# Optimization experiments

Measured on AMD Instinct MI355X. Metric: run time of the kernel, lower is better.

Reference implementation:

```python
import jax, jax.numpy as jnp
import numpy as np

B, S, D, H, FF = 2, 2048, 1024, 16, 4096
DK = D // H
MAX_SEQ_LEN = 2048
THETA = 10000.0
EPS = 1e-5


def _linear_init(key, out_f, in_f):
    std = (2.0 / (in_f + out_f)) ** 0.5
    return std * jax.random.truncated_normal(key, -3.0, 3.0, (out_f, in_f), dtype=jnp.float32)


def setup_inputs() -> dict:
    key = jax.random.key(0)
    ks = jax.random.split(key, 9)
    x = jax.random.normal(ks[0], (B, S, D), dtype=jnp.float32)
    token_positions = jnp.broadcast_to(jnp.arange(S, dtype=jnp.int32)[None, :], (B, S))
    return {
        "x": x,
        "wq": _linear_init(ks[1], D, D),
        "wk": _linear_init(ks[2], D, D),
        "wv": _linear_init(ks[3], D, D),
        "wo": _linear_init(ks[4], D, D),
        "w1": _linear_init(ks[5], FF, D),
        "w2": _linear_init(ks[6], D, FF),
        "w3": _linear_init(ks[7], FF, D),
        "g1": jnp.ones((D,), dtype=jnp.float32),
        "g2": jnp.ones((D,), dtype=jnp.float32),
        "token_positions": token_positions,
    }


def _rmsnorm(x, g):
    x32 = x.astype(jnp.float32)
    ms = jnp.sqrt(jnp.mean(x32 * x32, axis=-1, keepdims=True) + EPS)
    return ((x32 / ms) * g).astype(x.dtype)


def _rope(x, pos):
    # x: (B, H, S, DK); pos: (B, S)
    inv_freq = 1.0 / THETA ** (jnp.arange(0, DK, 2, dtype=jnp.float32) / DK)  # (DK/2,)
    freqs = pos.astype(jnp.float32)[..., None] * inv_freq  # (B, S, DK/2)
    cos = jnp.cos(freqs)[:, None, :, :]  # (B, 1, S, DK/2) broadcast over heads
    sin = jnp.sin(freqs)[:, None, :, :]
    x_real = x[..., 0::2]
    x_imag = x[..., 1::2]
    rot_real = x_real * cos - x_imag * sin
    rot_imag = x_real * sin + x_imag * cos
    return jnp.stack([rot_real, rot_imag], axis=-1).reshape(x.shape)


def reference(x, wq, wk, wv, wo, w1, w2, w3, g1, g2, token_positions):
    # --- attention sublayer ---
    h = _rmsnorm(x, g1)
    def proj(w):
        y = jnp.einsum('bsd,ed->bse', h, w)
        return y.reshape(B, S, H, DK).transpose(0, 2, 1, 3)  # (B,H,S,DK)
    Q = _rope(proj(wq), token_positions)
    K = _rope(proj(wk), token_positions)
    V = proj(wv)
    scores = jnp.einsum('bhqd,bhkd->bhqk', Q, K)  # (B,H,S,S) full matrix (naive)
    causal = jnp.tril(jnp.ones((S, S), dtype=bool))
    scores = jnp.where(causal, scores, -jnp.inf) / (DK ** 0.5)
    probs = jax.nn.softmax(scores, axis=-1)
    attn = jnp.einsum('bhqk,bhkd->bhqd', probs, V)
    attn = attn.transpose(0, 2, 1, 3).reshape(B, S, D)
    attn = jnp.einsum('bsd,ed->bse', attn, wo)
    y = x + attn
    # --- SwiGLU FFN sublayer ---
    h2 = _rmsnorm(y, g2)
    a = jnp.einsum('bsd,fd->bsf', h2, w1)
    gate = jnp.einsum('bsd,fd->bsf', h2, w3)
    ff = jnp.einsum('bsf,df->bsd', a * jax.nn.sigmoid(a) * gate, w2)
    return y + ff
```

## Files before the change

### kernel.cpp

```cpp
#include <hip/hip_runtime.h>
#include <hip/hip_bf16.h>

#define B_ 2
#define S_ 2048
#define D_ 1024
#define H_ 16
#define DK_ 64
#define FF_ 4096
#define M_ (B_ * S_)

typedef unsigned short u16;
typedef __bf16 bf16x8 __attribute__((ext_vector_type(8)));
typedef float f32x4 __attribute__((ext_vector_type(4)));
typedef u16 u16x4 __attribute__((ext_vector_type(4)));
typedef u16 u16x8 __attribute__((ext_vector_type(8)));

__device__ __forceinline__ u16 f2bf(float f) {
  __bf16 b = (__bf16)f;
  return __builtin_bit_cast(u16, b);
}
__device__ __forceinline__ float bf2f(u16 u) {
  __bf16 b = __builtin_bit_cast(__bf16, u);
  return (float)b;
}

__device__ __forceinline__ void async_lds16(const void* g, void* l) {
  __builtin_amdgcn_global_load_lds(
      (const __attribute__((address_space(1))) unsigned int*)g,
      (__attribute__((address_space(3))) unsigned int*)l, 16, 0, 0);
}

__device__ __forceinline__ void raw_barrier() {
  asm volatile("s_barrier" ::: "memory");
}
#define VMCNT_WAIT(n) asm volatile("s_waitcnt vmcnt(" #n ")" ::: "memory")

__global__ __launch_bounds__(256) void f2b_all(
    const float* __restrict__ wq, const float* __restrict__ wk,
    const float* __restrict__ wv, const float* __restrict__ wo,
    const float* __restrict__ w1, const float* __restrict__ w2,
    const float* __restrict__ w3, u16* __restrict__ wqkvb,
    u16* __restrict__ wob, u16* __restrict__ wb13, u16* __restrict__ w2b) {
  int i4 = blockIdx.x * 256 + threadIdx.x;
  const float* src;
  u16* dst;
  int off, oo;
  if (i4 < 262144) { src = wq; dst = wqkvb; off = i4; oo = off; }
  else if (i4 < 524288) { src = wk; dst = wqkvb + 1048576; off = i4 - 262144; oo = off; }
  else if (i4 < 786432) { src = wv; dst = wqkvb + 2097152; off = i4 - 524288; oo = off; }
  else if (i4 < 1048576) { src = wo; dst = wob; off = i4 - 786432; oo = off; }
  else if (i4 < 2097152) {
    src = w1; dst = wb13; off = i4 - 1048576;
    oo = ((off >> 8) * 2) * 256 + (off & 255);
  } else if (i4 < 3145728) { src = w2; dst = w2b; off = i4 - 2097152; oo = off; }
  else {
    src = w3; dst = wb13; off = i4 - 3145728;
    oo = ((off >> 8) * 2 + 1) * 256 + (off & 255);
  }
  float4 v = ((const float4*)src)[off];
  u16x4 o;
  o[0] = f2bf(v.x); o[1] = f2bf(v.y); o[2] = f2bf(v.z); o[3] = f2bf(v.w);
  *(u16x4*)(dst + (size_t)oo * 4) = o;
}

__global__ __launch_bounds__(256) void rmsnorm_k(const float* __restrict__ X,
                                                 const float* __restrict__ G,
                                                 u16* __restrict__ Out) {
  const int row = blockIdx.x, tid = threadIdx.x;
  const float4 xv = *(const float4*)(X + (size_t)row * D_ + tid * 4);
  float ss = xv.x * xv.x + xv.y * xv.y + xv.z * xv.z + xv.w * xv.w;
#pragma unroll
  for (int off = 1; off < 64; off <<= 1) ss += __shfl_xor(ss, off);
  __shared__ float red[4];
  if ((tid & 63) == 0) red[tid >> 6] = ss;
  __syncthreads();
  const float tot = red[0] + red[1] + red[2] + red[3];
  const float sc = rsqrtf(tot * (1.0f / D_) + 1e-5f);
  const float4 gv = *(const float4*)(G + tid * 4);
  u16x4 o;
  o[0] = f2bf(xv.x * sc * gv.x);
  o[1] = f2bf(xv.y * sc * gv.y);
  o[2] = f2bf(xv.z * sc * gv.z);
  o[3] = f2bf(xv.w * sc * gv.w);
  *(u16x4*)(Out + (size_t)row * D_ + tid * 4) = o;
}

__global__ __launch_bounds__(256) void rope2_k(unsigned int* __restrict__ Qb,
                                               unsigned int* __restrict__ Kb,
                                               const int* __restrict__ pos) {
  int idx = blockIdx.x * 256 + threadIdx.x;
  unsigned int* buf = Qb;
  float scale = 0.125f;
  if (idx >= 2097152) { buf = Kb; scale = 1.f; idx -= 2097152; }
  const int row = idx >> 9, p = idx & 511;
  const int i = p & 31;
  unsigned int v = buf[(size_t)row * 512 + p];
  const float xr = bf2f((u16)(v & 0xffffu));
  const float xi = bf2f((u16)(v >> 16));
  const float ang =
      (float)pos[row] * __expf(-(float)i * (9.210340371976184f / 32.0f));
  float sn, cs;
  sincosf(ang, &sn, &cs);
  const float orr = (xr * cs - xi * sn) * scale;
  const float oii = (xr * sn + xi * cs) * scale;
  buf[(size_t)row * 512 + p] =
      (unsigned int)f2bf(orr) | ((unsigned int)f2bf(oii) << 16);
}

__global__ __launch_bounds__(256) void transpose_v(const u16* __restrict__ V,
                                                   u16* __restrict__ Vt) {
  __shared__ __align__(16) u16 tile[32][64];
  const int tid = threadIdx.x;
  const int s0 = blockIdx.x * 32, bh = blockIdx.y, b = bh >> 4, h = bh & 15;
  {
    const int sr = tid >> 3, c = tid & 7;
    *(u16x8*)&tile[sr][c * 8] =
        *(const u16x8*)(V + (size_t)(b * S_ + s0 + sr) * D_ + h * DK_ + c * 8);
  }
  __syncthreads();
  {
    const int dk = tid >> 2, cs = tid & 3;
    u16x8 vv;
#pragma unroll
    for (int j = 0; j < 8; ++j) vv[j] = tile[cs * 8 + j][dk];
    *(u16x8*)(Vt + (size_t)(bh * DK_ + dk) * S_ + s0 + cs * 8) = vv;
  }
}

template <int EPI>
__global__ __launch_bounds__(512) void gemm8ph(const u16* __restrict__ A,
                                               const u16* __restrict__ Bw,
                                               void* __restrict__ Cout,
                                               const void* __restrict__ auxp,
                                               int N, int K) {
  constexpr int BM = 256, BN = 256, BK = 64;
  constexpr int CPR = BK / 8;
  constexpr int ACH = BM * CPR;
  __shared__ __align__(16) u16 As[2][BM * BK];
  __shared__ __align__(16) u16 Bs[2][BN * BK];
  const int tid = threadIdx.x, l = tid & 63, w = tid >> 6;
  const int gx = gridDim.x;
  const int nwg = gx * (int)gridDim.y;
  const int id = blockIdx.y * gx + blockIdx.x;
  const int swz = (id & 7) * (nwg >> 3) + (id >> 3);
  const int m0 = (swz / gx) * BM, n0 = (swz % gx) * BN;
  const int wm = (w >> 2) * 128, wn = (w & 3) * 64;
  const int lr = l & 15, lg = l >> 4;

  f32x4 acc[8][4] = {};

  auto STAGE_PART = [&](int bf, int k0, int i0, int i1) {
    for (int i = i0; i < i1; ++i) {
      const int s = i * 512 + tid;
      const int base = i * 512 + w * 64;
      if (base < ACH) {
        const int r = s / CPR, ch = s % CPR;
        async_lds16(A + (size_t)(m0 + r) * K + k0 + ((ch ^ (r & 7)) * 8),
                    (char*)As[bf] + base * 16);
      } else {
        const int s2 = s - ACH;
        const int r = s2 / CPR, ch = s2 % CPR;
        async_lds16(Bw + (size_t)(n0 + r) * K + k0 + ((ch ^ (r & 7)) * 8),
                    (char*)Bs[bf] + (base - ACH) * 16);
      }
    }
  };

  STAGE_PART(0, 0, 0, 8);
  VMCNT_WAIT(0);
  raw_barrier();
  int cur = 0;
  for (int k0 = 0; k0 < K; k0 += BK) {
    const bool more = (k0 + BK) < K;
    bf16x8 bfr[4];
#pragma unroll
    for (int ph = 0; ph < 4; ++ph) {
      const int kk = ph >> 1, iq = ph & 1;
      if (iq == 0) {
#pragma unroll
        for (int j = 0; j < 4; ++j) {
          const int row = wn + j * 16 + lr;
          bfr[j] = *(const bf16x8*)&Bs[cur][row * BK +
                                            (((kk * 4 + lg) ^ (row & 7)) * 8)];
        }
      }
      bf16x8 af[4];
#pragma unroll
      for (int i = 0; i < 4; ++i) {
        const int row = wm + (iq * 4 + i) * 16 + lr;
        af[i] = *(const bf16x8*)&As[cur][row * BK +
                                         (((kk * 4 + lg) ^ (row & 7)) * 8)];
      }
      if (more) {
        if (ph == 0) STAGE_PART(cur ^ 1, k0 + BK, 0, 3);
        else if (ph == 1) STAGE_PART(cur ^ 1, k0 + BK, 3, 6);
        else if (ph == 2) STAGE_PART(cur ^ 1, k0 + BK, 6, 8);
      }
      raw_barrier();
      __builtin_amdgcn_s_setprio(1);
#pragma unroll
      for (int i = 0; i < 4; ++i)
#pragma unroll
        for (int j = 0; j < 4; ++j)
          acc[iq * 4 + i][j] = __builtin_amdgcn_mfma_f32_16x16x32_bf16(
              af[i], bfr[j], acc[iq * 4 + i][j], 0, 0, 0);
      __builtin_amdgcn_s_setprio(0);
      if (ph < 3) raw_barrier();
    }
    if (more) {
      VMCNT_WAIT(0);
      raw_barrier();
    }
    cur ^= 1;
  }

#pragma unroll
  for (int i = 0; i < 8; ++i) {
#pragma unroll
    for (int j = 0; j < 4; ++j) {
#pragma unroll
      for (int t = 0; t < 4; ++t) {
        const int grow = m0 + wm + i * 16 + lg * 4 + t;
        const int gcol = n0 + wn + j * 16 + lr;
        const float v = acc[i][j][t];
        if (EPI == 0) {
          ((u16*)Cout)[(size_t)grow * N + gcol] = f2bf(v);
        } else if (EPI == 3) {
          u16* base = (u16*)Cout + (size_t)(gcol >> 10) * ((size_t)M_ * D_);
          base[(size_t)grow * D_ + (gcol & 1023)] = f2bf(v);
        } else {
          const float pv = __shfl_xor(v, 1);
          if (!(lr & 1)) {
            const float sw = v / (1.f + __expf(-v)) * pv;
            ((u16*)Cout)[(size_t)grow * FF_ + (gcol >> 1)] = f2bf(sw);
          }
        }
      }
    }
  }
}

template <int BM, int BN, int BK, int EPI>
__global__ __launch_bounds__(512) void gemm2ph(const u16* __restrict__ A,
                                               const u16* __restrict__ Bw,
                                               void* __restrict__ Cout,
                                               const void* __restrict__ auxp,
                                               int N, int K) {
  constexpr int CPR = BK / 8;
  constexpr int ACH = BM * CPR;
  constexpr int TCH = (BM + BN) * CPR;
  constexpr int MR = BM / 32, NR = BN / 64;
  static_assert(TCH / 512 == 8, "vmcnt(8) assumes 8 loads/thread per STAGE");
  __shared__ __align__(16) u16 As[2][BM * BK];
  __shared__ __align__(16) u16 Bs[2][BN * BK];
  const int tid = threadIdx.x, l = tid & 63, w = tid >> 6;
  const int gx = gridDim.x;
  const int nwg = gx * (int)gridDim.y;
  const int id = blockIdx.y * gx + blockIdx.x;
  const int swz = (id & 7) * (nwg >> 3) + (id >> 3);
  const int m0 = (swz / gx) * BM, n0 = (swz % gx) * BN;
  const int wm = (w >> 2) * (BM / 2), wn = (w & 3) * (BN / 4);
  const int lr = l & 15, lg = l >> 4;

  f32x4 acc[MR][NR] = {};

  auto STAGE = [&](int bf, int k0) {
#pragma unroll
    for (int i = 0; i < TCH / 512; ++i) {
      const int s = i * 512 + tid;
      const int base = i * 512 + w * 64;
      if (base < ACH) {
        const int r = s / CPR, ch = s % CPR;
        async_lds16(A + (size_t)(m0 + r) * K + k0 + ((ch ^ (r & 7)) * 8),
                    (char*)As[bf] + base * 16);
      } else {
        const int s2 = s - ACH;
        const int r = s2 / CPR, ch = s2 % CPR;
        async_lds16(Bw + (size_t)(n0 + r) * K + k0 + ((ch ^ (r & 7)) * 8),
                    (char*)Bs[bf] + (base - ACH) * 16);
      }
    }
  };

  STAGE(0, 0);
  int cur = 0;
  for (int k0 = 0; k0 < K; k0 += BK) {
    if (k0 + BK < K) {
      STAGE(cur ^ 1, k0 + BK);
      VMCNT_WAIT(8);
    } else {
      VMCNT_WAIT(0);
    }
    raw_barrier();
#pragma unroll
    for (int kk = 0; kk < BK / 32; ++kk) {
      bf16x8 af[MR], bfr[NR];
#pragma unroll
      for (int i = 0; i < MR; ++i) {
        const int row = wm + i * 16 + lr;
        af[i] = *(const bf16x8*)&As[cur][row * BK +
                                         (((kk * 4 + lg) ^ (row & 7)) * 8)];
      }
#pragma unroll
      for (int j = 0; j < NR; ++j) {
        const int row = wn + j * 16 + lr;
        bfr[j] = *(const bf16x8*)&Bs[cur][row * BK +
                                          (((kk * 4 + lg) ^ (row & 7)) * 8)];
      }
      __builtin_amdgcn_s_setprio(1);
#pragma unroll
      for (int i = 0; i < MR; ++i)
#pragma unroll
        for (int j = 0; j < NR; ++j)
          acc[i][j] = __builtin_amdgcn_mfma_f32_16x16x32_bf16(
              af[i], bfr[j], acc[i][j], 0, 0, 0);
      __builtin_amdgcn_s_setprio(0);
    }
    raw_barrier();
    cur ^= 1;
  }

#pragma unroll
  for (int i = 0; i < MR; ++i) {
#pragma unroll
    for (int j = 0; j < NR; ++j) {
#pragma unroll
      for (int t = 0; t < 4; ++t) {
        const int grow = m0 + wm + i * 16 + lg * 4 + t;
        const int gcol = n0 + wn + j * 16 + lr;
        const float v = acc[i][j][t];
        if (EPI == 0) {
          ((u16*)Cout)[(size_t)grow * N + gcol] = f2bf(v);
        } else if (EPI == 1) {
          const size_t idx = (size_t)grow * N + gcol;
          ((float*)Cout)[idx] = ((const float*)auxp)[idx] + v;
        }
      }
    }
  }
}

__global__ __launch_bounds__(256) void attn_fwd(const u16* __restrict__ Q,
                                                const u16* __restrict__ K,
                                                const u16* __restrict__ Vt,
                                                u16* __restrict__ O) {
  __shared__ __align__(16) u16 Ks[2][64 * 64];
  __shared__ __align__(16) u16 Vs[2][64 * 64];
  __shared__ __align__(16) u16 Ps[4][16 * 72];
  const int tid = threadIdx.x, l = tid & 63, w = tid >> 6;
  const int lr = l & 15, lg = l >> 4;
  const int bid = blockIdx.x;
  const int xcd = bid & 7, i = bid >> 3;
  const int bh = xcd * 4 + (i >> 5);
  const int qx = 31 - (i & 31);
  const int b = bh >> 4, h = bh & 15;
  const int q0w = qx * 64 + w * 16;

  const u16* Kb = K + (size_t)(b * S_) * D_ + h * DK_;
  const u16* Vb = Vt + (size_t)bh * DK_ * S_;

  bf16x8 aq[2];
  {
    const u16* qp = Q + (size_t)(b * S_ + q0w + lr) * D_ + h * DK_ + lg * 8;
    aq[0] = *(const bf16x8*)qp;
    aq[1] = *(const bf16x8*)(qp + 32);
  }
  f32x4 oacc[4] = {};
  float mrow[4], lrow[4];
#pragma unroll
  for (int t = 0; t < 4; ++t) { mrow[t] = -1e30f; lrow[t] = 0.f; }

  u16x8 ones_u;
#pragma unroll
  for (int j = 0; j < 8; ++j) ones_u[j] = 0x3F80;
  const bf16x8 ones = __builtin_bit_cast(bf16x8, ones_u);

  const int ntiles = qx + 1;

  auto STAGE = [&](int bf, int t) {
#pragma unroll
    for (int inst = 0; inst < 2; ++inst) {
      const int s = (w * 2 + inst) * 64 + l;
      const int r = s >> 3, ch = s & 7;
      const int chs = ch ^ (r & 7);
      async_lds16(Kb + (size_t)(t * 64 + r) * D_ + chs * 8,
                  (char*)Ks[bf] + (w * 2 + inst) * 1024);
      async_lds16(Vb + (size_t)r * S_ + t * 64 + chs * 8,
                  (char*)Vs[bf] + (w * 2 + inst) * 1024);
    }
  };

  STAGE(0, 0);
  int cur = 0;
  for (int it = 0; it < ntiles; ++it) {
    if (it + 1 < ntiles) {
      STAGE(cur ^ 1, it + 1);
      VMCNT_WAIT(4);
    } else {
      VMCNT_WAIT(0);
    }
    raw_barrier();
    f32x4 sf[4];
    __builtin_amdgcn_s_setprio(1);
#pragma unroll
    for (int n = 0; n < 4; ++n) {
      const int kvr = n * 16 + lr;
      f32x4 z = {};
      bf16x8 bk0 = *(const bf16x8*)&Ks[cur][kvr * 64 + ((lg ^ (kvr & 7)) * 8)];
      bf16x8 bk1 =
          *(const bf16x8*)&Ks[cur][kvr * 64 + (((4 + lg) ^ (kvr & 7)) * 8)];
      z = __builtin_amdgcn_mfma_f32_16x16x32_bf16(aq[0], bk0, z, 0, 0, 0);
      z = __builtin_amdgcn_mfma_f32_16x16x32_bf16(aq[1], bk1, z, 0, 0, 0);
      sf[n] = z;
    }
    __builtin_amdgcn_s_setprio(0);
    if (it < qx) {
      float fm[4];
      bool exc = false;
#pragma unroll
      for (int t = 0; t < 4; ++t) {
        fm[t] = fmaxf(fmaxf(sf[0][t], sf[1][t]), fmaxf(sf[2][t], sf[3][t]));
        exc |= fm[t] > mrow[t] + 8.f;
      }
      if (__any(exc)) {
#pragma unroll
        for (int t = 0; t < 4; ++t) {
          float mx = fm[t];
#pragma unroll
          for (int off = 1; off < 16; off <<= 1)
            mx = fmaxf(mx, __shfl_xor(mx, off));
          const float nm = fmaxf(mrow[t], mx);
          const float c = __expf(mrow[t] - nm);
          mrow[t] = nm;
          lrow[t] *= c;
#pragma unroll
          for (int d = 0; d < 4; ++d) oacc[d][t] *= c;
        }
      }
#pragma unroll
      for (int t = 0; t < 4; ++t)
#pragma unroll
        for (int n = 0; n < 4; ++n)
          Ps[w][(lg * 4 + t) * 72 + n * 16 + lr] =
              f2bf(__expf(sf[n][t] - mrow[t]));
    } else {
      const int kv0 = it * 64;
#pragma unroll
      for (int t = 0; t < 4; ++t) {
        const int qrow = q0w + lg * 4 + t;
        float v[4];
#pragma unroll
        for (int n = 0; n < 4; ++n)
          v[n] = (kv0 + n * 16 + lr <= qrow) ? sf[n][t] : -1e30f;
        float mx = fmaxf(fmaxf(v[0], v[1]), fmaxf(v[2], v[3]));
#pragma unroll
        for (int off = 1; off < 16; off <<= 1)
          mx = fmaxf(mx, __shfl_xor(mx, off));
        const float nm = fmaxf(mrow[t], mx);
        const float c = __expf(mrow[t] - nm);
        mrow[t] = nm;
        lrow[t] *= c;
#pragma unroll
        for (int d = 0; d < 4; ++d) oacc[d][t] *= c;
#pragma unroll
        for (int n = 0; n < 4; ++n)
          Ps[w][(lg * 4 + t) * 72 + n * 16 + lr] = f2bf(__expf(v[n] - nm));
      }
    }
    bf16x8 ap0 = *(const bf16x8*)&Ps[w][lr * 72 + lg * 8];
    bf16x8 ap1 = *(const bf16x8*)&Ps[w][lr * 72 + 32 + lg * 8];
    __builtin_amdgcn_s_setprio(1);
    f32x4 zs = {};
    zs = __builtin_amdgcn_mfma_f32_16x16x32_bf16(ap0, ones, zs, 0, 0, 0);
    zs = __builtin_amdgcn_mfma_f32_16x16x32_bf16(ap1, ones, zs, 0, 0, 0);
#pragma unroll
    for (int d = 0; d < 4; ++d) {
      const int row = d * 16 + lr;
      bf16x8 bv0 = *(const bf16x8*)&Vs[cur][row * 64 + ((lg ^ (row & 7)) * 8)];
      bf16x8 bv1 =
          *(const bf16x8*)&Vs[cur][row * 64 + (((4 + lg) ^ (row & 7)) * 8)];
      oacc[d] = __builtin_amdgcn_mfma_f32_16x16x32_bf16(ap0, bv0, oacc[d], 0, 0, 0);
      oacc[d] = __builtin_amdgcn_mfma_f32_16x16x32_bf16(ap1, bv1, oacc[d], 0, 0, 0);
    }
    __builtin_amdgcn_s_setprio(0);
#pragma unroll
    for (int t = 0; t < 4; ++t) lrow[t] += zs[t];
    raw_barrier();
    cur ^= 1;
  }
#pragma unroll
  for (int d = 0; d < 4; ++d) {
#pragma unroll
    for (int t = 0; t < 4; ++t) {
      const size_t idx =
          (size_t)(b * S_ + q0w + lg * 4 + t) * D_ + h * DK_ + d * 16 + lr;
      O[idx] = f2bf(oacc[d][t] / lrow[t]);
    }
  }
}

extern "C" void kernel_launch(void* const* d_in, const int* in_sizes, int n_in,
                              void* d_out, int out_size, void* d_ws,
                              size_t ws_size, hipStream_t stream) {
  (void)in_sizes; (void)n_in; (void)out_size; (void)ws_size;
  const float* x = (const float*)d_in[0];
  const float* wq = (const float*)d_in[1];
  const float* wk = (const float*)d_in[2];
  const float* wv = (const float*)d_in[3];
  const float* wo = (const float*)d_in[4];
  const float* w1 = (const float*)d_in[5];
  const float* w2 = (const float*)d_in[6];
  const float* w3 = (const float*)d_in[7];
  const float* g1 = (const float*)d_in[8];
  const float* g2 = (const float*)d_in[9];
  const int* tp = (const int*)d_in[10];
  float* out = (float*)d_out;

  char* ws = (char*)d_ws;
  const size_t MB = 1024u * 1024u;
  u16* wqkvb = (u16*)(ws + 0 * MB);
  u16* wob  = (u16*)(ws + 6 * MB);
  u16* wb13 = (u16*)(ws + 8 * MB);
  u16* w2b  = (u16*)(ws + 24 * MB);
  u16* hb   = (u16*)(ws + 32 * MB);
  float* yb = (float*)(ws + 40 * MB);
  u16* h2b  = (u16*)(ws + 56 * MB);
  u16* Qb   = (u16*)(ws + 64 * MB);
  u16* Kb   = (u16*)(ws + 72 * MB);
  u16* Vb   = (u16*)(ws + 80 * MB);
  u16* Vtb  = (u16*)(ws + 88 * MB);
  u16* ffb  = (u16*)(ws + 96 * MB);
  u16* aob  = hb;

  f2b_all<<<16384, 256, 0, stream>>>(wq, wk, wv, wo, w1, w2, w3, wqkvb, wob,
                                     wb13, w2b);

  rmsnorm_k<<<4096, 256, 0, stream>>>(x, g1, hb);

  gemm8ph<3><<<dim3(12, 16), 512, 0, stream>>>(hb, wqkvb, Qb, nullptr, 3072,
                                               1024);

  rope2_k<<<16384, 256, 0, stream>>>((unsigned int*)Qb, (unsigned int*)Kb, tp);
  transpose_v<<<dim3(64, 32), 256, 0, stream>>>(Vb, Vtb);

  attn_fwd<<<1024, 256, 0, stream>>>(Qb, Kb, Vtb, aob);

  gemm2ph<128, 128, 128, 1><<<dim3(8, 32), 512, 0, stream>>>(aob, wob, yb, x,
                                                             1024, 1024);
  rmsnorm_k<<<4096, 256, 0, stream>>>(yb, g2, h2b);

  gemm8ph<4><<<dim3(32, 16), 512, 0, stream>>>(h2b, wb13, ffb, nullptr, 8192,
                                               1024);
  gemm2ph<128, 128, 128, 1><<<dim3(8, 32), 512, 0, stream>>>(ffb, w2b, out, yb,
                                                             1024, 4096);
}
```

Baseline: 293.1 us.

## Block-interleave W1/W3 rows by 16 and issue all next-tile loads at once

The fused W1/W3 weight layout changes from alternating single rows to alternating 16-row blocks. The SwiGLU epilogue can then pair the a and gate values from adjacent accumulator tiles in the same lane, with no cross-lane shuffle, and every lane writes an output instead of half of them. The prefetch of the next K tile is also issued in one burst at phase 0 instead of being split across three phases. That burst may bunch memory traffic against the MFMA work, and the epilogue now depends on EPI==4 being the SwiGLU instantiation.

```diff
diff --git a/kernel.cpp b/kernel.cpp
--- a/kernel.cpp
+++ b/kernel.cpp
@@ -51,11 +51,13 @@
   else if (i4 < 1048576) { src = wo; dst = wob; off = i4 - 786432; oo = off; }
   else if (i4 < 2097152) {
     src = w1; dst = wb13; off = i4 - 1048576;
-    oo = ((off >> 8) * 2) * 256 + (off & 255);
+    const int r = off >> 8;
+    oo = (((r >> 4) * 32) + (r & 15)) * 256 + (off & 255);
   } else if (i4 < 3145728) { src = w2; dst = w2b; off = i4 - 2097152; oo = off; }
   else {
     src = w3; dst = wb13; off = i4 - 3145728;
-    oo = ((off >> 8) * 2 + 1) * 256 + (off & 255);
+    const int r = off >> 8;
+    oo = (((r >> 4) * 32) + 16 + (r & 15)) * 256 + (off & 255);
   }
   float4 v = ((const float4*)src)[off];
   u16x4 o;
@@ -149,8 +151,9 @@
 
   f32x4 acc[8][4] = {};
 
-  auto STAGE_PART = [&](int bf, int k0, int i0, int i1) {
-    for (int i = i0; i < i1; ++i) {
+  auto STAGE_ALL = [&](int bf, int k0) {
+#pragma unroll
+    for (int i = 0; i < 8; ++i) {
       const int s = i * 512 + tid;
       const int base = i * 512 + w * 64;
       if (base < ACH) {
@@ -166,7 +169,7 @@
     }
   };
 
-  STAGE_PART(0, 0, 0, 8);
+  STAGE_ALL(0, 0);
   VMCNT_WAIT(0);
   raw_barrier();
   int cur = 0;
@@ -191,11 +194,7 @@
         af[i] = *(const bf16x8*)&As[cur][row * BK +
                                          (((kk * 4 + lg) ^ (row & 7)) * 8)];
       }
-      if (more) {
-        if (ph == 0) STAGE_PART(cur ^ 1, k0 + BK, 0, 3);
-        else if (ph == 1) STAGE_PART(cur ^ 1, k0 + BK, 3, 6);
-        else if (ph == 2) STAGE_PART(cur ^ 1, k0 + BK, 6, 8);
-      }
+      if (more && ph == 0) STAGE_ALL(cur ^ 1, k0 + BK);
       raw_barrier();
       __builtin_amdgcn_s_setprio(1);
 #pragma unroll
@@ -228,12 +227,12 @@
         } else if (EPI == 3) {
           u16* base = (u16*)Cout + (size_t)(gcol >> 10) * ((size_t)M_ * D_);
           base[(size_t)grow * D_ + (gcol & 1023)] = f2bf(v);
-        } else {
-          const float pv = __shfl_xor(v, 1);
-          if (!(lr & 1)) {
-            const float sw = v / (1.f + __expf(-v)) * pv;
-            ((u16*)Cout)[(size_t)grow * FF_ + (gcol >> 1)] = f2bf(sw);
-          }
+        } else if (EPI == 4) {
+          if (j & 1) continue;
+          const float a = v, g = acc[i][j + 1][t];
+          const float sw = a / (1.f + __expf(-a)) * g;
+          const int ocol = ((n0 + wn) >> 1) + (j >> 1) * 16 + lr;
+          ((u16*)Cout)[(size_t)grow * FF_ + ocol] = f2bf(sw);
         }
       }
     }
```

Result: no change. 287.8 us (-1.8%).
